# Kernel optimization log

Hardware: AMD Instinct MI355X
Metric: run time of the kernel (lower is better)

The kernel has to match this reference:

```python
import jax, jax.numpy as jnp
import numpy as np
import math

DIM = 128
D_STATE = 16
D_CONV = 4
EXPAND = 2
LFS = 16            # last_feat_size -> H = W = 16, L = 256
IN_IMG = 512
IN_PC = 256
COMB = IN_IMG + IN_PC + 2          # 770
POOL_SCALES = [1, 5, 9, 13]        # arithmetic(1, 16, 4)
NPOOL = len(POOL_SCALES)
D_MODEL = DIM * NPOOL + COMB       # 1282
D_INNER = EXPAND * D_MODEL         # 2564
DT_RANK = math.ceil(D_MODEL / 16)  # 81
B = 64
H = W = LFS


def _ap_mat(insz, outsz):
    # PyTorch AdaptiveAvgPool2d bin weights as a (outsz, insz) matrix
    M = np.zeros((outsz, insz), np.float32)
    for i in range(outsz):
        s = (i * insz) // outsz
        e = -((-(i + 1) * insz) // outsz)  # ceil((i+1)*insz/outsz)
        M[i, s:e] = 1.0 / (e - s)
    return M


def _bl_mat(outsz, insz):
    # bilinear interpolation (align_corners=False) as (outsz, insz) matrix
    M = np.zeros((outsz, insz), np.float32)
    if insz == 1:
        M[:, 0] = 1.0
        return M
    for i in range(outsz):
        src = (i + 0.5) * insz / outsz - 0.5
        src = min(max(src, 0.0), insz - 1.0)
        i0 = int(np.floor(src))
        i1 = min(i0 + 1, insz - 1)
        f = src - i0
        M[i, i0] += 1.0 - f
        M[i, i1] += f
    return M


def setup_inputs():
    key = jax.random.key(0)
    ks = jax.random.split(key, 16)
    def n(k, sh, s=1.0):
        return jax.random.normal(k, sh, jnp.float32) * s
    return {
        'x': n(ks[0], (B, IN_IMG, H, W)),
        'pc_emb': n(ks[1], (B, IN_PC)),
        'conv_w': n(ks[2], (NPOOL, DIM, COMB), 0.05),          # 1x1 convs
        'bn_gamma': jnp.ones((NPOOL, DIM), jnp.float32),
        'bn_beta': jnp.zeros((NPOOL, DIM), jnp.float32),
        'bn_mean': n(ks[3], (NPOOL, DIM), 0.1),
        'bn_var': jax.random.uniform(ks[4], (NPOOL, DIM), jnp.float32, 0.5, 1.5),
        'in_proj_w': n(ks[5], (2 * D_INNER, D_MODEL), D_MODEL ** -0.5),
        'conv1d_w': n(ks[6], (D_INNER, 1, D_CONV), 0.3),       # depthwise causal conv
        'conv1d_b': n(ks[7], (D_INNER,), 0.1),
        'x_proj_w': n(ks[8], (DT_RANK + 2 * D_STATE, D_INNER), D_INNER ** -0.5),
        'dt_proj_w': n(ks[9], (D_INNER, DT_RANK), DT_RANK ** -0.5),
        'dt_proj_b': n(ks[10], (D_INNER,), 0.5) - 3.0,
        'A_log': jnp.log(jax.random.uniform(ks[11], (D_INNER, D_STATE), jnp.float32, 1.0, 16.0)),
        'D': jnp.ones((D_INNER,), jnp.float32),
        'out_proj_w': n(ks[12], (D_MODEL, D_INNER), D_INNER ** -0.5),
    }


def _ppm(x, pc_emb, conv_w, bn_gamma, bn_beta, bn_mean, bn_var):
    Bn = x.shape[0]
    xx = np.linspace(-0.3, 0.3, LFS, dtype=np.float32)
    g = np.stack(np.meshgrid(xx, xx)).reshape(2, LFS, LFS)
    grid = jnp.broadcast_to(jnp.asarray(g)[None], (Bn, 2, H, W))
    pc = jnp.broadcast_to(pc_emb[:, :, None, None], (Bn, IN_PC, H, W))
    comb = jnp.concatenate([x, grid, pc], axis=1)  # (B, COMB, H, W)

    def cbr(i, t):  # 1x1 conv -> BN(eval) -> ReLU6
        y = jnp.einsum('bchw,dc->bdhw', t, conv_w[i])
        inv = jax.lax.rsqrt(bn_var[i] + 1e-5) * bn_gamma[i]
        y = y * inv[None, :, None, None] + (bn_beta[i] - bn_mean[i] * inv)[None, :, None, None]
        return jnp.clip(y, 0.0, 6.0)

    outs = [comb]
    # pool layer 0: ConvBNReLU then AdaptiveAvgPool2d(1); bilinear from 1x1 = broadcast
    y0 = cbr(0, comb).mean(axis=(2, 3), keepdims=True)
    outs.append(jnp.broadcast_to(y0, (Bn, DIM, H, W)))
    for i, s in enumerate(POOL_SCALES[1:], start=1):
        Mp = jnp.asarray(_ap_mat(H, s))
        pooled = jnp.einsum('oh,bchw,pw->bcop', Mp, comb, Mp)  # adaptive avg pool
        y = cbr(i, pooled)
        Mu = jnp.asarray(_bl_mat(H, s))
        outs.append(jnp.einsum('oh,bchw,pw->bcop', Mu, y, Mu))  # bilinear upsample
    return jnp.concatenate(outs, axis=1)  # (B, D_MODEL, H, W)


def _mamba(seq, in_proj_w, conv1d_w, conv1d_b, x_proj_w, dt_proj_w, dt_proj_b, A_log, D, out_proj_w):
    # seq: (B, L, d_model)
    xz = seq @ in_proj_w.T                       # (B, L, 2*d_inner)
    u, z = jnp.split(xz, 2, axis=-1)
    uc = jnp.transpose(u, (0, 2, 1))             # (B, d_inner, L)
    uc = jax.lax.conv_general_dilated(uc, conv1d_w, (1,), [(D_CONV - 1, 0)],
                                      feature_group_count=D_INNER) + conv1d_b[None, :, None]
    u = jax.nn.silu(jnp.transpose(uc, (0, 2, 1)))  # (B, L, d_inner)
    dbl = u @ x_proj_w.T
    dt, Bm, Cm = jnp.split(dbl, [DT_RANK, DT_RANK + D_STATE], axis=-1)
    dt = jax.nn.softplus(dt @ dt_proj_w.T + dt_proj_b)  # (B, L, d_inner)
    A = -jnp.exp(A_log)                                 # (d_inner, d_state)

    def step(h, inp):
        dt_t, B_t, C_t, u_t = inp                # (B,d_inner) (B,N) (B,N) (B,d_inner)
        dA = jnp.exp(dt_t[..., None] * A)        # (B, d_inner, N)
        h = dA * h + (dt_t * u_t)[..., None] * B_t[:, None, :]
        y = jnp.einsum('bdn,bn->bd', h, C_t)
        return h, y

    h0 = jnp.zeros((seq.shape[0], D_INNER, D_STATE), seq.dtype)
    xs = (jnp.moveaxis(dt, 1, 0), jnp.moveaxis(Bm, 1, 0),
          jnp.moveaxis(Cm, 1, 0), jnp.moveaxis(u, 1, 0))
    _, ys = jax.lax.scan(step, h0, xs)
    y = jnp.moveaxis(ys, 0, 1) + u * D
    y = y * jax.nn.silu(z)
    return y @ out_proj_w.T                      # (B, L, d_model)


def reference(x, pc_emb, conv_w, bn_gamma, bn_beta, bn_mean, bn_var,
              in_proj_w, conv1d_w, conv1d_b, x_proj_w, dt_proj_w, dt_proj_b,
              A_log, D, out_proj_w):
    Bn = x.shape[0]
    feat = _ppm(x, pc_emb, conv_w, bn_gamma, bn_beta, bn_mean, bn_var)
    chs = feat.shape[1]
    seq = jnp.transpose(feat.reshape(Bn, chs, H * W), (0, 2, 1))  # b (h w) c
    y = _mamba(seq, in_proj_w, conv1d_w, conv1d_b, x_proj_w,
               dt_proj_w, dt_proj_b, A_log, D, out_proj_w)
    return jnp.transpose(y, (0, 2, 1)).reshape(Bn, chs, H, W)
```

## Files before the change

### kernel.cpp

```cpp
#include <hip/hip_runtime.h>
#include <hip/hip_bf16.h>
#include <math.h>

#define H_ 16
#define W_ 16
#define L_ 256
#define BATCH 64
#define CIMG 512
#define CPC 256
#define COMB_ 770
#define DIMC 128
#define DMODEL 1282
#define DINNER 2564
#define DXZ 5128
#define DTRANK 81
#define NSTATE 16
#define NPOS 275

#define KP_IN 928
#define KBASE 384
#define KP_OUT 2592
#define KP_DT 96
#define NPAD_IN 5248
#define NPAD_OUT 1408
#define NPAD_X 128
#define NPAD_DT 2688
#define XSPLIT 9

typedef __attribute__((ext_vector_type(8))) short short8;
typedef __attribute__((ext_vector_type(4))) float f32x4;

__device__ __forceinline__ float comb_val(const float* __restrict__ x,
                                          const float* __restrict__ pc,
                                          int bg, int c, int h, int w) {
  if (c < CIMG)    return x[(((size_t)bg * CIMG + c) << 8) + (h << 4) + w];
  if (c == CIMG)   return -0.3f + 0.04f * (float)w;
  if (c == CIMG+1) return -0.3f + 0.04f * (float)h;
  return pc[bg * CPC + (c - (CIMG + 2))];
}

__device__ __forceinline__ void split_bf16(float v, unsigned short& h, unsigned short& l) {
  __hip_bfloat16 hb = __float2bfloat16(v);
  h = __builtin_bit_cast(unsigned short, hb);
  float r = v - __bfloat162float(hb);
  __hip_bfloat16 lb = __float2bfloat16(r);
  l = __builtin_bit_cast(unsigned short, lb);
}

__device__ __forceinline__ float bf16_val(unsigned short u) {
  return __bfloat162float(__builtin_bit_cast(__hip_bfloat16, u));
}

__device__ __forceinline__ void idx_to_scale(int idx, int& s, int& o, int& p, int& base) {
  if (idx < 25)       { s = 5;  base = 0; }
  else if (idx < 106) { s = 9;  base = 25; }
  else                { s = 13; base = 106; }
  int r = idx - base;
  o = r / s; p = r - o * s;
}

__global__ __launch_bounds__(256) void wsplit_kernel(
    const float* __restrict__ W, int N, int K,
    unsigned short* __restrict__ Wh, unsigned short* __restrict__ Wl, int Kp) {
  int k = blockIdx.x * 256 + threadIdx.x;
  if (k >= Kp) return;
  int n = blockIdx.y;
  float v = (n < N && k < K) ? W[(size_t)n * K + k] : 0.f;
  unsigned short h, l;
  split_bf16(v, h, l);
  Wh[(size_t)n * Kp + k] = h;
  Wl[(size_t)n * Kp + k] = l;
}

__global__ __launch_bounds__(256) void wsplit_main_kernel(
    const float* __restrict__ W,
    unsigned short* __restrict__ Wh, unsigned short* __restrict__ Wl) {
  int k = blockIdx.x * 256 + threadIdx.x;
  if (k >= KP_IN) return;
  int n = blockIdx.y;
  float v = 0.f;
  if (n < DXZ && k < 898) {
    int src = (k < 514) ? k : k + 384;
    v = W[(size_t)n * DMODEL + src];
  }
  unsigned short h, l;
  split_bf16(v, h, l);
  Wh[(size_t)n * KP_IN + k] = h;
  Wl[(size_t)n * KP_IN + k] = l;
}

__global__ __launch_bounds__(256) void wsplit_base_kernel(
    const float* __restrict__ W,
    unsigned short* __restrict__ Wh, unsigned short* __restrict__ Wl) {
  int k = blockIdx.x * 256 + threadIdx.x;
  if (k >= KBASE) return;
  int n = blockIdx.y;
  float v = (n < DXZ) ? W[(size_t)n * DMODEL + 514 + k] : 0.f;
  unsigned short h, l;
  split_bf16(v, h, l);
  Wh[(size_t)n * KBASE + k] = h;
  Wl[(size_t)n * KBASE + k] = l;
}

__global__ __launch_bounds__(128) void wt_kernel(
    const float* __restrict__ cw, float* __restrict__ Wt) {
  int c = blockIdx.x, i = blockIdx.y, d = threadIdx.x;
  Wt[((size_t)i * COMB_ + c) * DIMC + d] = cw[((size_t)i * DIMC + d) * COMB_ + c];
}

__global__ __launch_bounds__(256) void pool_kernel(
    const float* __restrict__ x, const float* __restrict__ pc,
    float* __restrict__ P, int b0) {
  int t = blockIdx.x * 256 + threadIdx.x;
  if (t >= COMB_ * NPOS) return;
  int bl = blockIdx.y;
  int bg = b0 + bl;
  int c = t / NPOS;
  int idx = t - c * NPOS;
  int s, o, p, base; idx_to_scale(idx, s, o, p, base);
  int hs = (o * 16) / s, he = ((o + 1) * 16 + s - 1) / s;
  int ws2 = (p * 16) / s, we = ((p + 1) * 16 + s - 1) / s;
  float sum = 0.f;
  for (int h = hs; h < he; h++)
    for (int w = ws2; w < we; w++)
      sum += comb_val(x, pc, bg, c, h, w);
  P[((size_t)bl * COMB_ + c) * NPOS + idx] = sum / (float)((he - hs) * (we - ws2));
}

__global__ __launch_bounds__(256) void cbr_pool_kernel(
    const float* __restrict__ P, const float* __restrict__ Wt,
    const float* __restrict__ gamma, const float* __restrict__ beta,
    const float* __restrict__ mean, const float* __restrict__ var,
    float* __restrict__ Y) {
  int tno = blockIdx.x, bl = blockIdx.y;
  int i, idx0, cnt;
  if (tno == 0)      { i = 0; idx0 = 0;                cnt = 25; }
  else if (tno < 4)  { i = 1; idx0 = 25 + (tno-1)*32;  cnt = min(32, 106 - idx0); }
  else               { i = 2; idx0 = 106 + (tno-4)*32; cnt = min(32, 275 - idx0); }
  __shared__ float Ps[64][32];
  __shared__ float Ws[64][128];
  int t = threadIdx.x;
  int dg = t & 31, ig = t >> 5;
  int d0 = dg << 2, ii0 = ig << 2;
  float acc[4][4] = {};
  for (int c0 = 0; c0 < COMB_; c0 += 64) {
    int cend = min(64, COMB_ - c0);
    for (int e = t; e < 64 * 32; e += 256) {
      int cc = e >> 5, ii = e & 31;
      float v = 0.f;
      if (cc < cend && ii < cnt)
        v = P[((size_t)bl * COMB_ + c0 + cc) * NPOS + idx0 + ii];
      Ps[cc][ii] = v;
    }
    for (int e = t; e < 64 * 128; e += 256) {
      int cc = e >> 7, dd = e & 127;
      Ws[cc][dd] = (cc < cend) ? Wt[((size_t)(i + 1) * COMB_ + c0 + cc) * DIMC + dd] : 0.f;
    }
    __syncthreads();
    for (int cc = 0; cc < 64; cc++) {
      f32x4 wv = *(const f32x4*)&Ws[cc][d0];
      f32x4 pv = *(const f32x4*)&Ps[cc][ii0];
      #pragma unroll
      for (int di = 0; di < 4; di++)
        #pragma unroll
        for (int ki = 0; ki < 4; ki++)
          acc[di][ki] += wv[di] * pv[ki];
    }
    __syncthreads();
  }
  #pragma unroll
  for (int di = 0; di < 4; di++) {
    int bi = (i + 1) * DIMC + d0 + di;
    float inv = rsqrtf(var[bi] + 1e-5f) * gamma[bi];
    float bs = beta[bi] - mean[bi] * inv;
    #pragma unroll
    for (int ki = 0; ki < 4; ki++) {
      int io = ii0 + ki;
      if (io < cnt) {
        float v = fminf(fmaxf(acc[di][ki] * inv + bs, 0.f), 6.f);
        Y[((size_t)bl * NPOS + idx0 + io) * DIMC + d0 + di] = v;
      }
    }
  }
}

__global__ __launch_bounds__(256) void cbr0a_kernel(
    const float* __restrict__ x, const float* __restrict__ pc,
    const float* __restrict__ Wt, float* __restrict__ y0c) {
  int tile = blockIdx.x, bl = blockIdx.y;
  int lt = tile & 3, cg = tile >> 2;
  int cbeg = (cg * COMB_) >> 2, cend_ = ((cg + 1) * COMB_) >> 2;
  __shared__ float Cs[64][64];
  __shared__ float Ws[64][128];
  int t = threadIdx.x;
  int dg = t & 31, lg = t >> 5;
  int d0 = dg << 2, l0 = lg << 3;
  float acc[4][8] = {};
  for (int c0 = cbeg; c0 < cend_; c0 += 64) {
    int cn = min(64, cend_ - c0);
    for (int e = t; e < 64 * 64; e += 256) {
      int cc = e >> 6, ll = e & 63;
      float v = 0.f;
      if (cc < cn) {
        int l = lt * 64 + ll;
        v = comb_val(x, pc, bl, c0 + cc, l >> 4, l & 15);
      }
      Cs[cc][ll] = v;
    }
    for (int e = t; e < 64 * 128; e += 256) {
      int cc = e >> 7, dd = e & 127;
      Ws[cc][dd] = (cc < cn) ? Wt[(size_t)(c0 + cc) * DIMC + dd] : 0.f;
    }
    __syncthreads();
    for (int cc = 0; cc < 64; cc++) {
      f32x4 wv = *(const f32x4*)&Ws[cc][d0];
      f32x4 pa = *(const f32x4*)&Cs[cc][l0];
      f32x4 pb = *(const f32x4*)&Cs[cc][l0 + 4];
      #pragma unroll
      for (int di = 0; di < 4; di++) {
        #pragma unroll
        for (int li = 0; li < 4; li++) {
          acc[di][li]     += wv[di] * pa[li];
          acc[di][li + 4] += wv[di] * pb[li];
        }
      }
    }
    __syncthreads();
  }
  #pragma unroll
  for (int di = 0; di < 4; di++)
    #pragma unroll
    for (int li = 0; li < 8; li++)
      y0c[(((size_t)bl * 4 + cg) * 256 + lt * 64 + l0 + li) * DIMC + d0 + di] =
          acc[di][li];
}

__global__ __launch_bounds__(256) void cbr0b_kernel(
    const float* __restrict__ y0c,
    const float* __restrict__ gamma, const float* __restrict__ beta,
    const float* __restrict__ mean, const float* __restrict__ var,
    float* __restrict__ y0s) {
  int bl = blockIdx.x;
  int t = threadIdx.x;
  int d = t & 127, lh = t >> 7;
  float inv = rsqrtf(var[d] + 1e-5f) * gamma[d];
  float bs = beta[d] - mean[d] * inv;
  float s = 0.f;
  size_t cgs = (size_t)256 * DIMC;
  for (int l = lh * 128; l < lh * 128 + 128; l++) {
    size_t base = (((size_t)bl * 4) * 256 + l) * DIMC + d;
    float v = y0c[base] + y0c[base + cgs] + y0c[base + 2 * cgs] + y0c[base + 3 * cgs];
    v = v * inv + bs;
    s += fminf(fmaxf(v, 0.f), 6.f);
  }
  __shared__ float red[256];
  red[t] = s;
  __syncthreads();
  if (t < 128) y0s[bl * DIMC + t] = red[t] + red[t + 128];
}

__global__ __launch_bounds__(256) void pcy0_kernel(
    const float* __restrict__ pc, const float* __restrict__ y0s,
    unsigned short* __restrict__ Abh, unsigned short* __restrict__ Abl) {
  int k = blockIdx.x * 256 + threadIdx.x;
  if (k >= KBASE) return;
  int row = blockIdx.y;
  float v = 0.f;
  if (row < BATCH) {
    if (k < CPC) v = pc[row * CPC + k];
    else v = y0s[(size_t)row * DIMC + (k - CPC)] * (1.f / 256.f);
  }
  unsigned short h, l;
  split_bf16(v, h, l);
  Abh[(size_t)row * KBASE + k] = h;
  Abl[(size_t)row * KBASE + k] = l;
}

__global__ __launch_bounds__(256) void seq_x_kernel(
    const float* __restrict__ x,
    unsigned short* __restrict__ seqh, unsigned short* __restrict__ seql, int b0) {
  int ct = blockIdx.x, ltile = blockIdx.y, bl = blockIdx.z;
  int bg = b0 + bl;
  __shared__ float Ct[64][65];
  int t = threadIdx.x;
  int c0 = ct << 6, l0 = ltile << 6;
  for (int e = t; e < 64 * 64; e += 256) {
    int cc = e >> 6, ll = e & 63;
    Ct[ll][cc] = x[(((size_t)bg * CIMG + c0 + cc) << 8) + l0 + ll];
  }
  __syncthreads();
  int r = t >> 2, cq = (t & 3) << 4;
  size_t rb = ((size_t)bl * L_ + l0 + r) * KP_IN + c0 + cq;
  short8 h0, h1, lo0, lo1;
  #pragma unroll
  for (int k = 0; k < 8; k++) {
    unsigned short hh, ll;
    split_bf16(Ct[r][cq + k], hh, ll);
    h0[k] = (short)hh; lo0[k] = (short)ll;
  }
  #pragma unroll
  for (int k = 0; k < 8; k++) {
    unsigned short hh, ll;
    split_bf16(Ct[r][cq + 8 + k], hh, ll);
    h1[k] = (short)hh; lo1[k] = (short)ll;
  }
  *(short8*)&seqh[rb]     = h0;
  *(short8*)&seqh[rb + 8] = h1;
  *(short8*)&seql[rb]     = lo0;
  *(short8*)&seql[rb + 8] = lo1;
}

__global__ __launch_bounds__(256) void seq_rest_kernel(
    const float* __restrict__ x, const float* __restrict__ pc,
    const float* __restrict__ Y,
    unsigned short* __restrict__ seqh, unsigned short* __restrict__ seql, int b0) {
  int l = blockIdx.x, bl = blockIdx.y, bg = b0 + bl;
  int h = l >> 4, w = l & 15;
  size_t rb = ((size_t)bl * L_ + l) * KP_IN;
  for (int c = 512 + threadIdx.x; c < KP_IN; c += 256) {
    float v;
    if (c < CIMG + 2) {
      v = comb_val(x, pc, bg, c, h, w);
    } else if (c < 898) {
      int cc = c - 514;
      int si = cc >> 7;
      int d = cc & 127;
      int s    = (si == 0) ? 5 : ((si == 1) ? 9 : 13);
      int base = (si == 0) ? 0 : ((si == 1) ? 25 : 106);
      float srch = (h + 0.5f) * (float)s * (1.f / 16.f) - 0.5f;
      srch = fminf(fmaxf(srch, 0.f), (float)(s - 1));
      int o0 = (int)floorf(srch);
      float fh = srch - (float)o0;
      int o1 = min(o0 + 1, s - 1);
      float srcw = (w + 0.5f) * (float)s * (1.f / 16.f) - 0.5f;
      srcw = fminf(fmaxf(srcw, 0.f), (float)(s - 1));
      int p0 = (int)floorf(srcw);
      float fw = srcw - (float)p0;
      int p1 = min(p0 + 1, s - 1);
      const float* Yb = &Y[((size_t)bg * NPOS + base) * DIMC + d];
      float v00 = Yb[(size_t)(o0 * s + p0) * DIMC];
      float v01 = Yb[(size_t)(o0 * s + p1) * DIMC];
      float v10 = Yb[(size_t)(o1 * s + p0) * DIMC];
      float v11 = Yb[(size_t)(o1 * s + p1) * DIMC];
      v = (1.f - fh) * ((1.f - fw) * v00 + fw * v01)
        +        fh  * ((1.f - fw) * v10 + fw * v11);
    } else {
      v = 0.f;
    }
    unsigned short hh, ll;
    split_bf16(v, hh, ll);
    seqh[rb + c] = hh;
    seql[rb + c] = ll;
  }
}

__global__ __launch_bounds__(256) void mfma_gemm_kernel(
    const unsigned short* __restrict__ Ah, const unsigned short* __restrict__ Al, int Kp,
    const unsigned short* __restrict__ Bh, const unsigned short* __restrict__ Bl,
    float* __restrict__ C, int ldc, int M, int N, int mode,
    const float* __restrict__ bias,
    float* __restrict__ outT, int b0, size_t czstr) {
  __shared__ __align__(16) unsigned short Ash[128 * 32];
  __shared__ __align__(16) unsigned short Asl[128 * 32];
  __shared__ __align__(16) unsigned short Bsh[128 * 32];
  __shared__ __align__(16) unsigned short Bsl[128 * 32];
  int tid = threadIdx.x;
  int lane = tid & 63;
  int wave = tid >> 6;

  int kn = Kp / (int)gridDim.z;
  int kbeg = (int)blockIdx.z * kn;
  int kend = kbeg + kn;
  C += (size_t)blockIdx.z * czstr;

  int gx = gridDim.x, gy = gridDim.y;
  int lin = blockIdx.y * gx + blockIdx.x;
  int total = gx * gy;
  int mt, nt;
  if ((total & 7) == 0) {
    int vid = (lin & 7) * (total >> 3) + (lin >> 3);
    mt = vid % gy; nt = vid / gy;
  } else {
    mt = blockIdx.y; nt = blockIdx.x;
  }
  int m0 = mt << 7, n0 = nt << 7;
  int wm = (wave & 1) << 6, wn = (wave >> 1) << 6;
  f32x4 acc[4][4] = {};
  int mrow = lane & 15;
  int kx = (((lane >> 4) ^ ((lane >> 2) & 3)) << 3);

  for (int k0 = kbeg; k0 < kend; k0 += 32) {
    #pragma unroll
    for (int j = 0; j < 2; j++) {
      int c = (j << 8) + tid;
      int r = c >> 2;
      int kc = (((c & 3) ^ ((r >> 2) & 3)) << 3);
      size_t ga = (size_t)(m0 + r) * Kp + k0 + kc;
      size_t gb = (size_t)(n0 + r) * Kp + k0 + kc;
      __builtin_amdgcn_global_load_lds(
          (const __attribute__((address_space(1))) unsigned int*)(Ah + ga),
          (__attribute__((address_space(3))) unsigned int*)(&Ash[c << 3]), 16, 0, 0);
      __builtin_amdgcn_global_load_lds(
          (const __attribute__((address_space(1))) unsigned int*)(Al + ga),
          (__attribute__((address_space(3))) unsigned int*)(&Asl[c << 3]), 16, 0, 0);
      __builtin_amdgcn_global_load_lds(
          (const __attribute__((address_space(1))) unsigned int*)(Bh + gb),
          (__attribute__((address_space(3))) unsigned int*)(&Bsh[c << 3]), 16, 0, 0);
      __builtin_amdgcn_global_load_lds(
          (const __attribute__((address_space(1))) unsigned int*)(Bl + gb),
          (__attribute__((address_space(3))) unsigned int*)(&Bsl[c << 3]), 16, 0, 0);
    }
    __syncthreads();
    short8 ah[4], al[4], bh[4], blo[4];
    #pragma unroll
    for (int i = 0; i < 4; i++) {
      int ro = (wm + (i << 4) + mrow) * 32 + kx;
      ah[i] = *(const short8*)&Ash[ro];
      al[i] = *(const short8*)&Asl[ro];
    }
    #pragma unroll
    for (int j = 0; j < 4; j++) {
      int ro = (wn + (j << 4) + mrow) * 32 + kx;
      bh[j]  = *(const short8*)&Bsh[ro];
      blo[j] = *(const short8*)&Bsl[ro];
    }
    #pragma unroll
    for (int i = 0; i < 4; i++)
      #pragma unroll
      for (int j = 0; j < 4; j++) {
        acc[i][j] = __builtin_amdgcn_mfma_f32_16x16x32_bf16(ah[i], bh[j],  acc[i][j], 0, 0, 0);
        acc[i][j] = __builtin_amdgcn_mfma_f32_16x16x32_bf16(ah[i], blo[j], acc[i][j], 0, 0, 0);
        acc[i][j] = __builtin_amdgcn_mfma_f32_16x16x32_bf16(al[i], bh[j],  acc[i][j], 0, 0, 0);
      }
    __syncthreads();
  }

  int n_l = lane & 15, m_l = (lane >> 4) << 2;
  #pragma unroll
  for (int i = 0; i < 4; i++) {
    int gm0 = m0 + wm + (i << 4) + m_l;
    #pragma unroll
    for (int j = 0; j < 4; j++) {
      int gn = n0 + wn + (j << 4) + n_l;
      if (gn >= N) continue;
      if (mode == 2) {
        int bb = b0 + (gm0 >> 8), l0 = gm0 & 255;
        *(f32x4*)&outT[(((size_t)bb * DMODEL + gn) << 8) + l0] = acc[i][j];
      } else if (mode == 1) {
        float bv = bias[gn];
        #pragma unroll
        for (int r = 0; r < 4; r++) {
          float vv = acc[i][j][r] + bv;
          vv = (vv > 20.f) ? vv : log1pf(expf(vv));
          C[(size_t)(gm0 + r) * ldc + gn] = vv;
        }
      } else if (mode == 3) {
        float bv = bias[(size_t)(b0 + (gm0 >> 8)) * DXZ + gn];
        if (gn < DINNER) {
          #pragma unroll
          for (int r = 0; r < 4; r++)
            C[(size_t)(gm0 + r) * DINNER + gn] = acc[i][j][r] + bv;
        } else {
          int g2 = gn - DINNER;
          #pragma unroll
          for (int r = 0; r < 4; r++)
            outT[(size_t)(gm0 + r) * DINNER + g2] = acc[i][j][r] + bv;
        }
      } else {
        #pragma unroll
        for (int r = 0; r < 4; r++)
          C[(size_t)(gm0 + r) * ldc + gn] = acc[i][j][r];
      }
    }
  }
}

__global__ __launch_bounds__(256) void conv1d_kernel(
    const float* __restrict__ U, const float* __restrict__ cw,
    const float* __restrict__ cb,
    unsigned short* __restrict__ vh, unsigned short* __restrict__ vl) {
  int d = blockIdx.x * 256 + threadIdx.x;
  if (d >= KP_OUT) return;
  int m0 = blockIdx.y << 2;
  if (d >= DINNER) {
    #pragma unroll
    for (int q = 0; q < 4; q++) {
      size_t o = (size_t)(m0 + q) * KP_OUT + d;
      vh[o] = 0; vl[o] = 0;
    }
    return;
  }
  int bbase = m0 & ~255;
  float xr[7];
  #pragma unroll
  for (int k = 0; k < 7; k++) {
    int r = m0 - 3 + k;
    xr[k] = (r >= bbase) ? U[(size_t)r * DINNER + d] : 0.f;
  }
  float w0 = cw[d * 4], w1 = cw[d * 4 + 1], w2 = cw[d * 4 + 2], w3 = cw[d * 4 + 3];
  float b = cb[d];
  #pragma unroll
  for (int q = 0; q < 4; q++) {
    float acc = b + w0 * xr[q] + w1 * xr[q + 1] + w2 * xr[q + 2] + w3 * xr[q + 3];
    float s = acc / (1.f + __expf(-acc));
    unsigned short hh, llv;
    split_bf16(s, hh, llv);
    size_t o = (size_t)(m0 + q) * KP_OUT + d;
    vh[o] = hh; vl[o] = llv;
  }
}

__global__ __launch_bounds__(256) void split_bc_kernel(
    const float* __restrict__ dbl, size_t zstr,
    unsigned short* __restrict__ dth, unsigned short* __restrict__ dtl,
    float* __restrict__ bcs, int Mtot) {
  int t = blockIdx.x * 256 + threadIdx.x;
  int m = t >> 7, k = t & 127;
  if (m >= Mtot) return;
  const float* p = dbl + (size_t)m * 128;
  if (k < KP_DT) {
    float v = 0.f;
    if (k < DTRANK) {
      #pragma unroll
      for (int q = 0; q < XSPLIT; q++) v += p[(size_t)q * zstr + k];
    }
    unsigned short h, l;
    split_bf16(v, h, l);
    dth[(size_t)m * KP_DT + k] = h;
    dtl[(size_t)m * KP_DT + k] = l;
  } else {
    int n = k - KP_DT;
    float v = 0.f;
    #pragma unroll
    for (int q = 0; q < XSPLIT; q++) v += p[(size_t)q * zstr + DTRANK + n];
    bcs[(size_t)m * 32 + n] = v;
  }
}

__global__ __launch_bounds__(256) void scan_kernel(
    const float* __restrict__ dtv,
    const unsigned short* __restrict__ vh, const unsigned short* __restrict__ vl,
    const float* __restrict__ Z,
    const float* __restrict__ bcs, const float* __restrict__ A_log,
    const float* __restrict__ Dv,
    unsigned short* __restrict__ yh, unsigned short* __restrict__ yl) {
  int dl = threadIdx.x & 63;
  int s  = threadIdx.x >> 6;
  int d  = (blockIdx.x << 6) + dl;
  int bl = blockIdx.y;
  bool valid = d < DINNER;
  bool wout  = d < KP_OUT;
  int de = valid ? d : (DINNER - 1);
  __shared__ float Sh[3][64][NSTATE];
  __shared__ float Sp[3][64][NSTATE];
  float A[NSTATE], h[NSTATE];
  #pragma unroll
  for (int n = 0; n < NSTATE; n++) {
    A[n] = -__expf(A_log[de * NSTATE + n]);
    h[n] = 0.f;
  }
  float Dd = Dv[de];
  size_t mb = (size_t)bl * L_ + (s << 6);
  if (s < 3) {
    float sdt = 0.f;
    for (int i = 0; i < 64; i++) {
      size_t m = mb + i;
      float dt = dtv[m * DINNER + de];
      float uu = bf16_val(vh[m * KP_OUT + de]) + bf16_val(vl[m * KP_OUT + de]);
      const f32x4* bp = (const f32x4*)&bcs[m * 32];
      f32x4 b4a = bp[0], b4b = bp[1], b4c = bp[2], b4d = bp[3];
      float du = dt * uu;
      sdt += dt;
      #pragma unroll
      for (int n = 0; n < NSTATE; n++) {
        float bv = (n < 4) ? b4a[n & 3] : (n < 8) ? b4b[n & 3]
                 : (n < 12) ? b4c[n & 3] : b4d[n & 3];
        h[n] = __expf(dt * A[n]) * h[n] + du * bv;
      }
    }
    #pragma unroll
    for (int n = 0; n < NSTATE; n++) {
      Sh[s][dl][n] = h[n];
      Sp[s][dl][n] = __expf(A[n] * sdt);
    }
  }
  __syncthreads();
  #pragma unroll
  for (int n = 0; n < NSTATE; n++) h[n] = 0.f;
  for (int t = 0; t < s; t++)
    #pragma unroll
    for (int n = 0; n < NSTATE; n++)
      h[n] = Sp[t][dl][n] * h[n] + Sh[t][dl][n];
  for (int i = 0; i < 64; i++) {
    size_t m = mb + i;
    float dt = dtv[m * DINNER + de];
    float uu = bf16_val(vh[m * KP_OUT + de]) + bf16_val(vl[m * KP_OUT + de]);
    float zz = Z[m * DINNER + de];
    const f32x4* bp = (const f32x4*)&bcs[m * 32];
    f32x4 b4a = bp[0], b4b = bp[1], b4c = bp[2], b4d = bp[3];
    f32x4 c4a = bp[4], c4b = bp[5], c4c = bp[6], c4d = bp[7];
    float du = dt * uu;
    float y = 0.f;
    #pragma unroll
    for (int n = 0; n < NSTATE; n++) {
      float bv = (n < 4) ? b4a[n & 3] : (n < 8) ? b4b[n & 3]
               : (n < 12) ? b4c[n & 3] : b4d[n & 3];
      float cv = (n < 4) ? c4a[n & 3] : (n < 8) ? c4b[n & 3]
               : (n < 12) ? c4c[n & 3] : c4d[n & 3];
      h[n] = __expf(dt * A[n]) * h[n] + du * bv;
      y += h[n] * cv;
    }
    float val = (y + uu * Dd) * (zz / (1.f + __expf(-zz)));
    if (!valid) val = 0.f;
    if (wout) {
      unsigned short hh, ll;
      split_bf16(val, hh, ll);
      yh[m * KP_OUT + d] = hh;
      yl[m * KP_OUT + d] = ll;
    }
  }
}

extern "C" void kernel_launch(void* const* d_in, const int* in_sizes, int n_in,
                              void* d_out, int out_size, void* d_ws, size_t ws_size,
                              hipStream_t stream) {
  const float* x         = (const float*)d_in[0];
  const float* pc        = (const float*)d_in[1];
  const float* conv_w    = (const float*)d_in[2];
  const float* bn_gamma  = (const float*)d_in[3];
  const float* bn_beta   = (const float*)d_in[4];
  const float* bn_mean   = (const float*)d_in[5];
  const float* bn_var    = (const float*)d_in[6];
  const float* in_proj_w = (const float*)d_in[7];
  const float* conv1d_w  = (const float*)d_in[8];
  const float* conv1d_b  = (const float*)d_in[9];
  const float* x_proj_w  = (const float*)d_in[10];
  const float* dt_proj_w = (const float*)d_in[11];
  const float* dt_proj_b = (const float*)d_in[12];
  const float* A_log     = (const float*)d_in[13];
  const float* Dvec      = (const float*)d_in[14];
  const float* out_proj_w= (const float*)d_in[15];
  float* out = (float*)d_out;

  auto al = [](size_t vv) { return (vv + 255) & ~(size_t)255; };

  size_t w_in_sz  = al((size_t)NPAD_IN * KP_IN * 2);
  size_t w_b_sz   = al((size_t)NPAD_IN * KBASE * 2);
  size_t w_out_sz = al((size_t)NPAD_OUT * KP_OUT * 2);
  size_t w_x_sz   = al((size_t)NPAD_X * KP_OUT * 2);
  size_t w_d_sz   = al((size_t)NPAD_DT * KP_DT * 2);
  size_t wt_sz    = al((size_t)4 * COMB_ * DIMC * 4);
  size_t y0s_sz   = al((size_t)BATCH * DIMC * 4);
  size_t ab_sz    = al((size_t)128 * KBASE * 2);
  size_t cb_sz    = al((size_t)128 * DXZ * 4);
  size_t yf_sz    = al((size_t)BATCH * NPOS * DIMC * 4);
  size_t p_sz     = al((size_t)BATCH * COMB_ * NPOS * 4);
  size_t y0c_sz   = al((size_t)BATCH * 4 * 256 * DIMC * 4);

  char* base = (char*)d_ws;
  size_t off = 0;
  auto take = [&](size_t sz) { void* r = base + off; off += sz; return r; };
  unsigned short* Wih = (unsigned short*)take(w_in_sz);
  unsigned short* Wil = (unsigned short*)take(w_in_sz);
  unsigned short* Wbh = (unsigned short*)take(w_b_sz);
  unsigned short* Wbl = (unsigned short*)take(w_b_sz);
  unsigned short* Woh = (unsigned short*)take(w_out_sz);
  unsigned short* Wol = (unsigned short*)take(w_out_sz);
  unsigned short* Wxh = (unsigned short*)take(w_x_sz);
  unsigned short* Wxl = (unsigned short*)take(w_x_sz);
  unsigned short* Wdh = (unsigned short*)take(w_d_sz);
  unsigned short* Wdl = (unsigned short*)take(w_d_sz);
  float* Wt    = (float*)take(wt_sz);
  float* y0s   = (float*)take(y0s_sz);
  unsigned short* Abh = (unsigned short*)take(ab_sz);
  unsigned short* Abl = (unsigned short*)take(ab_sz);
  float* Cbase = (float*)take(cb_sz);
  float* Yf    = (float*)take(yf_sz);
  char* arena  = base + off;

  size_t pro_need = p_sz + y0c_sz;
  auto chunk = [&](int bc) -> size_t {
    size_t Mcb = (size_t)bc * L_;
    size_t hyb = al(Mcb * KP_OUT * 2);
    size_t s = 2 * hyb
             + 2 * al(Mcb * DINNER * 4)
             + 2 * al(Mcb * KP_OUT * 2)
             + al((size_t)XSPLIT * Mcb * 128 * 4)
             + al(Mcb * 32 * 4)
             + 2 * al(Mcb * KP_DT * 2);
    return s < pro_need ? pro_need : s;
  };
  int Bc = 64;
  while (Bc > 1 && off + chunk(Bc) > ws_size) Bc >>= 1;

  size_t Mc = (size_t)Bc * L_;
  size_t hy = al(Mc * KP_OUT * 2);
  size_t zstr = Mc * 128;
  size_t aoff = 0;
  auto takeA = [&](size_t sz) { void* r = arena + aoff; aoff += sz; return r; };
  float* P   = (float*)arena;
  float* y0c = (float*)(arena + p_sz);
  unsigned short* seqh = (unsigned short*)takeA(hy);
  unsigned short* seql = (unsigned short*)takeA(hy);
  float* U   = (float*)takeA(al(Mc * DINNER * 4));
  float* Z   = (float*)takeA(al(Mc * DINNER * 4));
  unsigned short* vhb = (unsigned short*)takeA(al(Mc * KP_OUT * 2));
  unsigned short* vlb = (unsigned short*)takeA(al(Mc * KP_OUT * 2));
  float* dblb = (float*)takeA(al((size_t)XSPLIT * Mc * 128 * 4));
  float* bcs  = (float*)takeA(al(Mc * 32 * 4));
  unsigned short* dth = (unsigned short*)takeA(al(Mc * KP_DT * 2));
  unsigned short* dtl = (unsigned short*)takeA(al(Mc * KP_DT * 2));
  unsigned short* yhb = seqh;
  unsigned short* ylb = seql;
  float* dtb = U;

  wsplit_main_kernel<<<dim3((KP_IN + 255) / 256, NPAD_IN), 256, 0, stream>>>(
      in_proj_w, Wih, Wil);
  wsplit_base_kernel<<<dim3((KBASE + 255) / 256, NPAD_IN), 256, 0, stream>>>(
      in_proj_w, Wbh, Wbl);
  wsplit_kernel<<<dim3((KP_OUT + 255) / 256, NPAD_OUT), 256, 0, stream>>>(
      out_proj_w, DMODEL, DINNER, Woh, Wol, KP_OUT);
  wsplit_kernel<<<dim3((KP_OUT + 255) / 256, NPAD_X), 256, 0, stream>>>(
      x_proj_w, DTRANK + 2 * NSTATE, DINNER, Wxh, Wxl, KP_OUT);
  wsplit_kernel<<<dim3((KP_DT + 255) / 256, NPAD_DT), 256, 0, stream>>>(
      dt_proj_w, DINNER, DTRANK, Wdh, Wdl, KP_DT);
  wt_kernel<<<dim3(COMB_, 4), 128, 0, stream>>>(conv_w, Wt);

  pool_kernel<<<dim3((COMB_ * NPOS + 255) / 256, BATCH), 256, 0, stream>>>(x, pc, P, 0);
  cbr_pool_kernel<<<dim3(10, BATCH), 256, 0, stream>>>(P, Wt, bn_gamma, bn_beta,
                                                       bn_mean, bn_var, Yf);
  cbr0a_kernel<<<dim3(16, BATCH), 256, 0, stream>>>(x, pc, Wt, y0c);
  cbr0b_kernel<<<dim3(BATCH), 256, 0, stream>>>(y0c, bn_gamma, bn_beta,
                                                bn_mean, bn_var, y0s);
  pcy0_kernel<<<dim3((KBASE + 255) / 256, 128), 256, 0, stream>>>(pc, y0s, Abh, Abl);
  mfma_gemm_kernel<<<dim3(NPAD_IN / 128, 1, 1), 256, 0, stream>>>(
      Abh, Abl, KBASE, Wbh, Wbl, Cbase, DXZ, 128, DXZ, 0, nullptr, nullptr, 0, 0);

  for (int b0 = 0; b0 < BATCH; b0 += Bc) {
    int Mci = (int)Mc;
    seq_x_kernel<<<dim3(8, 4, Bc), 256, 0, stream>>>(x, seqh, seql, b0);
    seq_rest_kernel<<<dim3(L_, Bc), 256, 0, stream>>>(x, pc, Yf, seqh, seql, b0);
    mfma_gemm_kernel<<<dim3(NPAD_IN / 128, Mci / 128, 1), 256, 0, stream>>>(
        seqh, seql, KP_IN, Wih, Wil, U, DINNER, Mci, DXZ, 3, Cbase, Z, b0, 0);
    conv1d_kernel<<<dim3((KP_OUT + 255) / 256, Mci / 4), 256, 0, stream>>>(
        U, conv1d_w, conv1d_b, vhb, vlb);
    mfma_gemm_kernel<<<dim3(1, Mci / 128, XSPLIT), 256, 0, stream>>>(
        vhb, vlb, KP_OUT, Wxh, Wxl, dblb, 128, Mci, DTRANK + 2 * NSTATE, 0,
        nullptr, nullptr, 0, zstr);
    split_bc_kernel<<<dim3(Mci / 2), 256, 0, stream>>>(dblb, zstr, dth, dtl, bcs, Mci);
    mfma_gemm_kernel<<<dim3(NPAD_DT / 128, Mci / 128, 1), 256, 0, stream>>>(
        dth, dtl, KP_DT, Wdh, Wdl, dtb, DINNER, Mci, DINNER, 1, dt_proj_b,
        nullptr, 0, 0);
    scan_kernel<<<dim3(41, Bc), 256, 0, stream>>>(
        dtb, vhb, vlb, Z, bcs, A_log, Dvec, yhb, ylb);
    mfma_gemm_kernel<<<dim3(NPAD_OUT / 128, Mci / 128, 1), 256, 0, stream>>>(
        yhb, ylb, KP_OUT, Woh, Wol, nullptr, 0, Mci, DMODEL, 2, nullptr, out, b0, 0);
  }
}
```

Measured before the change: 3.143 ms.

## Double-buffer LDS tiles in split-bf16 MFMA GEMM to overlap loads with compute

The GEMM kernel now keeps two LDS stages and issues the global-to-LDS loads for the next K tile before running the MFMAs on the current one. The aim is to hide global memory latency behind the matrix math. This doubles LDS use to 64 KB per block, which may lower occupancy. There is also a correctness risk: only one barrier per iteration, and async global_load_lds completion may not be waited on (vmcnt) before the next tile is read.

```diff
diff --git a/kernel.cpp b/kernel.cpp
--- a/kernel.cpp
+++ b/kernel.cpp
@@ -360,36 +360,33 @@
     float* __restrict__ C, int ldc, int M, int N, int mode,
     const float* __restrict__ bias,
     float* __restrict__ outT, int b0, size_t czstr) {
-  __shared__ __align__(16) unsigned short Ash[128 * 32];
-  __shared__ __align__(16) unsigned short Asl[128 * 32];
-  __shared__ __align__(16) unsigned short Bsh[128 * 32];
-  __shared__ __align__(16) unsigned short Bsl[128 * 32];
+  __shared__ __align__(16) unsigned short Sbuf[2][4][128 * 32];
   int tid = threadIdx.x;
   int lane = tid & 63;
   int wave = tid >> 6;
 
   int kn = Kp / (int)gridDim.z;
   int kbeg = (int)blockIdx.z * kn;
-  int kend = kbeg + kn;
+  int nt = kn >> 5;
   C += (size_t)blockIdx.z * czstr;
 
   int gx = gridDim.x, gy = gridDim.y;
   int lin = blockIdx.y * gx + blockIdx.x;
   int total = gx * gy;
-  int mt, nt;
+  int mt, nt_;
   if ((total & 7) == 0) {
     int vid = (lin & 7) * (total >> 3) + (lin >> 3);
-    mt = vid % gy; nt = vid / gy;
+    mt = vid % gy; nt_ = vid / gy;
   } else {
-    mt = blockIdx.y; nt = blockIdx.x;
-  }
-  int m0 = mt << 7, n0 = nt << 7;
+    mt = blockIdx.y; nt_ = blockIdx.x;
+  }
+  int m0 = mt << 7, n0 = nt_ << 7;
   int wm = (wave & 1) << 6, wn = (wave >> 1) << 6;
   f32x4 acc[4][4] = {};
   int mrow = lane & 15;
   int kx = (((lane >> 4) ^ ((lane >> 2) & 3)) << 3);
 
-  for (int k0 = kbeg; k0 < kend; k0 += 32) {
+  auto STAGE = [&](int ph, int k0) {
     #pragma unroll
     for (int j = 0; j < 2; j++) {
       int c = (j << 8) + tid;
@@ -399,30 +396,36 @@
       size_t gb = (size_t)(n0 + r) * Kp + k0 + kc;
       __builtin_amdgcn_global_load_lds(
           (const __attribute__((address_space(1))) unsigned int*)(Ah + ga),
-          (__attribute__((address_space(3))) unsigned int*)(&Ash[c << 3]), 16, 0, 0);
+          (__attribute__((address_space(3))) unsigned int*)(&Sbuf[ph][0][c << 3]), 16, 0, 0);
       __builtin_amdgcn_global_load_lds(
           (const __attribute__((address_space(1))) unsigned int*)(Al + ga),
-          (__attribute__((address_space(3))) unsigned int*)(&Asl[c << 3]), 16, 0, 0);
+          (__attribute__((address_space(3))) unsigned int*)(&Sbuf[ph][1][c << 3]), 16, 0, 0);
       __builtin_amdgcn_global_load_lds(
           (const __attribute__((address_space(1))) unsigned int*)(Bh + gb),
-          (__attribute__((address_space(3))) unsigned int*)(&Bsh[c << 3]), 16, 0, 0);
+          (__attribute__((address_space(3))) unsigned int*)(&Sbuf[ph][2][c << 3]), 16, 0, 0);
       __builtin_amdgcn_global_load_lds(
           (const __attribute__((address_space(1))) unsigned int*)(Bl + gb),
-          (__attribute__((address_space(3))) unsigned int*)(&Bsl[c << 3]), 16, 0, 0);
-    }
-    __syncthreads();
+          (__attribute__((address_space(3))) unsigned int*)(&Sbuf[ph][3][c << 3]), 16, 0, 0);
+    }
+  };
+
+  STAGE(0, kbeg);
+  __syncthreads();
+  int cur = 0;
+  for (int t = 0; t < nt; t++) {
+    if (t + 1 < nt) STAGE(cur ^ 1, kbeg + ((t + 1) << 5));
     short8 ah[4], al[4], bh[4], blo[4];
     #pragma unroll
     for (int i = 0; i < 4; i++) {
       int ro = (wm + (i << 4) + mrow) * 32 + kx;
-      ah[i] = *(const short8*)&Ash[ro];
-      al[i] = *(const short8*)&Asl[ro];
+      ah[i] = *(const short8*)&Sbuf[cur][0][ro];
+      al[i] = *(const short8*)&Sbuf[cur][1][ro];
     }
     #pragma unroll
     for (int j = 0; j < 4; j++) {
       int ro = (wn + (j << 4) + mrow) * 32 + kx;
-      bh[j]  = *(const short8*)&Bsh[ro];
-      blo[j] = *(const short8*)&Bsl[ro];
+      bh[j]  = *(const short8*)&Sbuf[cur][2][ro];
+      blo[j] = *(const short8*)&Sbuf[cur][3][ro];
     }
     #pragma unroll
     for (int i = 0; i < 4; i++)
@@ -433,6 +436,7 @@
         acc[i][j] = __builtin_amdgcn_mfma_f32_16x16x32_bf16(al[i], bh[j],  acc[i][j], 0, 0, 0);
       }
     __syncthreads();
+    cur ^= 1;
   }
 
   int n_l = lane & 15, m_l = (lane >> 4) << 2;
```

Result: faster. 2.631 ms (-16.3%).
